# Performance work log

Measured on AMD Instinct MI355X. Metric: run time of the kernel, lower is better.

Reference implementation:

```python
import jax, jax.numpy as jnp
import numpy as np

B, T, N, D = 16, 16, 256, 384  # batch, timesteps, patches, feature dim
QDIM = 384                      # query_dim
TEMP = 1.0                      # temperature
TOPK = 16                       # topk_k
EPS = 1e-8


def setup_inputs() -> dict:
    key = jax.random.key(0)
    k1, k2, k3, k4, k5, k6 = jax.random.split(key, 6)
    queries = jax.random.normal(k1, (B, T, QDIM), dtype=jnp.float32)
    patch_features = jax.random.normal(k2, (B, T, N, D), dtype=jnp.float32)
    # encoder.query_input_proj: Linear(query_dim -> D)
    W_in = jax.random.normal(k3, (QDIM, D), dtype=jnp.float32) / np.sqrt(QDIM)
    b_in = jax.random.normal(k4, (D,), dtype=jnp.float32) * 0.01
    # encoder.query_output_proj: Linear(D -> dino_dim)
    W_out = jax.random.normal(k5, (D, QDIM), dtype=jnp.float32) / np.sqrt(D)
    b_out = jax.random.normal(k6, (QDIM,), dtype=jnp.float32) * 0.01
    return {"queries": queries, "patch_features": patch_features,
            "W_in": W_in, "b_in": b_in, "W_out": W_out, "b_out": b_out}


def reference(queries, patch_features, W_in, b_in, W_out, b_out):
    # q_proj: [B,T,D]
    q_proj = jnp.einsum('btq,qd->btd', queries, W_in) + b_in
    # scores: [B,T,N]
    scores = jnp.einsum('btd,btnd->btn', q_proj, patch_features) / TEMP
    attn = jax.nn.softmax(scores, axis=-1)
    # top-k hard mask + renormalize
    k = min(TOPK, N)
    vals, idx = jax.lax.top_k(attn, k)                     # [B,T,k]
    bi = jnp.arange(B)[:, None, None]
    ti = jnp.arange(T)[None, :, None]
    attn_hard = jnp.zeros_like(attn).at[bi, ti, idx].set(vals)
    attn = attn_hard / (attn_hard.sum(axis=-1, keepdims=True) + EPS)
    # weighted sum over patches: [B,T,D]
    out = jnp.einsum('btn,btnd->btd', attn, patch_features)
    out = jnp.einsum('btd,dq->btq', out, W_out) + b_out    # [B,T,QDIM]
    return out
```

## Files before the change

kernel.cpp:

```cpp
#include <hip/hip_runtime.h>
#include <math.h>

#define B_  16
#define T_  16
#define N_  256
#define D_  384
#define Q_  384
#define K_  16
#define BT_ (B_ * T_)

__global__ __launch_bounds__(1024, 4)
void fused_kernel(const float* __restrict__ queries,
                  const float* __restrict__ patch,
                  const float* __restrict__ W_in,
                  const float* __restrict__ b_in,
                  const float* __restrict__ W_out,
                  const float* __restrict__ b_out,
                  float* __restrict__ out)
{
    const int bt   = blockIdx.x;
    const int tid  = threadIdx.x;
    const int lane = tid & 63;
    const int wave = tid >> 6;

    __shared__ __align__(16) float s_q[Q_];
    __shared__ __align__(16) float s_qp[D_];
    __shared__ __align__(16) float s_sc[N_];
    __shared__ __align__(16) int   s_cnt4[N_][4];
    __shared__ float s_red[4];
    __shared__ float s_red2[4][2];
    __shared__ float s_w[K_];
    __shared__ int   s_ix[K_];
    __shared__ __align__(16) float s_p8[8][D_];
    __shared__ __align__(16) float s_od[D_];

    const float* __restrict__ ptile = patch + (size_t)bt * N_ * D_;
    float* s_flat = &s_p8[0][0];

    if (tid < Q_) s_q[tid] = queries[(size_t)bt * Q_ + tid];
    __syncthreads();

    const int g16 = lane >> 4;
    const int sl  = lane & 15;
    const int n0  = wave * 4 + g16;

    float4 A[6], Bu[6], C[6];

#define LOADROW(dst, it) {                                                     \
        const float* pr = ptile + (size_t)(n0 + (it) * 64) * D_;               \
        _Pragma("unroll")                                                      \
        for (int c = 0; c < 6; ++c)                                            \
            dst[c] = *reinterpret_cast<const float4*>(pr + c * 64 + 4 * sl); }

#define DOTSTORE(src, it) {                                                    \
        float p = 0.f;                                                         \
        _Pragma("unroll")                                                      \
        for (int c = 0; c < 6; ++c)                                            \
            p += src[c].x * qv[c].x + src[c].y * qv[c].y                       \
               + src[c].z * qv[c].z + src[c].w * qv[c].w;                      \
        _Pragma("unroll")                                                      \
        for (int off = 8; off; off >>= 1) p += __shfl_xor(p, off, 16);         \
        if (sl == 0) s_sc[n0 + (it) * 64] = p; }

    LOADROW(A, 0)
    LOADROW(Bu, 1)
    LOADROW(C, 2)
    __builtin_amdgcn_sched_barrier(0);

    if (tid < 768) {
        const int s = tid / 96;
        const int g = tid % 96;
        float4 acc = {0.f, 0.f, 0.f, 0.f};
        const float* wp = W_in + (size_t)(s * 48) * D_ + 4 * g;
        #pragma unroll 4
        for (int qq = 0; qq < 48; ++qq) {
            const float4 w = *reinterpret_cast<const float4*>(wp + (size_t)qq * D_);
            const float qs = s_q[s * 48 + qq];
            acc.x += qs * w.x; acc.y += qs * w.y;
            acc.z += qs * w.z; acc.w += qs * w.w;
        }
        *reinterpret_cast<float4*>(&s_p8[s][4 * g]) = acc;
    }
    __syncthreads();
    if (tid < D_) {
        float v = b_in[tid];
        #pragma unroll
        for (int s = 0; s < 8; ++s) v += s_p8[s][tid];
        s_qp[tid] = v;
    }
    __syncthreads();

    {
        const float4* s_qp4 = reinterpret_cast<const float4*>(s_qp);
        float4 qv[6];
        #pragma unroll
        for (int c = 0; c < 6; ++c) qv[c] = s_qp4[c * 16 + sl];

        DOTSTORE(A, 0)
        LOADROW(A, 3)
        DOTSTORE(Bu, 1)
        DOTSTORE(C, 2)
        DOTSTORE(A, 3)
    }
#undef LOADROW
#undef DOTSTORE
    __syncthreads();

    if (tid < N_) {
        float v = s_sc[tid];
        #pragma unroll
        for (int off = 32; off; off >>= 1) v = fmaxf(v, __shfl_xor(v, off));
        if (lane == 0) s_red[wave] = v;
    }
    {
        const int i   = tid >> 2;
        const int sub = tid & 3;
        const float si = s_sc[i];
        const float4* s_sc4 = reinterpret_cast<const float4*>(s_sc);
        int c = 0;
        #pragma unroll
        for (int jj = 0; jj < 16; ++jj) {
            const int jr = (jj + sub * 4) & 15;
            const float4 v = s_sc4[sub * 16 + jr];
            const int j0 = sub * 64 + jr * 4;
            c += (int)(v.x > si) | ((int)(v.x == si) & (int)((j0 + 0) < i));
            c += (int)(v.y > si) | ((int)(v.y == si) & (int)((j0 + 1) < i));
            c += (int)(v.z > si) | ((int)(v.z == si) & (int)((j0 + 2) < i));
            c += (int)(v.w > si) | ((int)(v.w == si) & (int)((j0 + 3) < i));
        }
        s_cnt4[i][sub] = c;
    }
    __syncthreads();

    float e = 0.f;
    int   cnt = N_;
    if (tid < N_) {
        const float mx = fmaxf(fmaxf(s_red[0], s_red[1]), fmaxf(s_red[2], s_red[3]));
        const int4 c4 = reinterpret_cast<const int4*>(s_cnt4)[tid];
        cnt = c4.x + c4.y + c4.z + c4.w;
        e = __expf(s_sc[tid] - mx);

        float z  = e;
        float sk = (cnt < K_) ? e : 0.f;
        #pragma unroll
        for (int off = 32; off; off >>= 1) {
            z  += __shfl_xor(z, off);
            sk += __shfl_xor(sk, off);
        }
        if (lane == 0) { s_red2[wave][0] = z; s_red2[wave][1] = sk; }
    }
    __syncthreads();

    {
        const float Z  = s_red2[0][0] + s_red2[1][0] + s_red2[2][0] + s_red2[3][0];
        const float SK = s_red2[0][1] + s_red2[1][1] + s_red2[2][1] + s_red2[3][1];
        const float inv = 1.f / (SK + 1e-8f * Z);
        if (tid < N_ && cnt < K_) {
            s_ix[cnt] = tid;
            s_w[cnt]  = e * inv;
        }
    }
    __syncthreads();

    if (tid < 2 * D_) {
        const int half = tid >= D_;
        const int d    = tid - half * D_;
        const int j0   = half * (K_ / 2);
        float acc = 0.f;
        #pragma unroll
        for (int j = j0; j < j0 + K_ / 2; ++j)
            acc += s_w[j] * ptile[(size_t)s_ix[j] * D_ + d];
        s_flat[tid] = acc;
    }
    __syncthreads();
    if (tid < D_) s_od[tid] = s_flat[tid] + s_flat[tid + D_];
    __syncthreads();

    if (tid < 768) {
        const int s = tid / 96;
        const int g = tid % 96;
        float4 acc = {0.f, 0.f, 0.f, 0.f};
        const float* wp = W_out + (size_t)(s * 48) * Q_ + 4 * g;
        #pragma unroll 4
        for (int dd = 0; dd < 48; ++dd) {
            const float4 w = *reinterpret_cast<const float4*>(wp + (size_t)dd * Q_);
            const float ov = s_od[s * 48 + dd];
            acc.x += ov * w.x; acc.y += ov * w.y;
            acc.z += ov * w.z; acc.w += ov * w.w;
        }
        *reinterpret_cast<float4*>(&s_p8[s][4 * g]) = acc;
    }
    __syncthreads();
    if (tid < Q_) {
        float v = b_out[tid];
        #pragma unroll
        for (int s = 0; s < 8; ++s) v += s_p8[s][tid];
        out[(size_t)bt * Q_ + tid] = v;
    }
}

extern "C" void kernel_launch(void* const* d_in, const int* in_sizes, int n_in,
                              void* d_out, int out_size, void* d_ws, size_t ws_size,
                              hipStream_t stream) {
    const float* queries = (const float*)d_in[0];
    const float* patch   = (const float*)d_in[1];
    const float* W_in    = (const float*)d_in[2];
    const float* b_in    = (const float*)d_in[3];
    const float* W_out   = (const float*)d_in[4];
    const float* b_out   = (const float*)d_in[5];
    float* out = (float*)d_out;

    fused_kernel<<<dim3(BT_), dim3(1024), 0, stream>>>(
        queries, patch, W_in, b_in, W_out, b_out, out);
}
```

Baseline: 34.46 us.

## Pack top-k rank keys, prefetch W_out during gather, single-pass weighted sum

Scores are encoded as order-preserving unsigned keys with the patch index in the low 8 bits, so the rank count uses one unsigned compare instead of a compare plus tie-break. The first eight W_out rows are prefetched into registers before the top-k gather so their latency overlaps it. The gather now runs on 384 threads with four independent accumulators, removing one shared-memory reduction and a barrier. Truncating the low 8 mantissa bits can change the selection when scores are nearly tied, and the prefetch raises register pressure.

```diff
diff --git a/kernel.cpp b/kernel.cpp
--- a/kernel.cpp
+++ b/kernel.cpp
@@ -26,6 +26,7 @@
     __shared__ __align__(16) float s_q[Q_];
     __shared__ __align__(16) float s_qp[D_];
     __shared__ __align__(16) float s_sc[N_];
+    __shared__ __align__(16) unsigned s_ku[N_];
     __shared__ __align__(16) int   s_cnt4[N_][4];
     __shared__ float s_red[4];
     __shared__ float s_red2[4][2];
@@ -35,7 +36,6 @@
     __shared__ __align__(16) float s_od[D_];
 
     const float* __restrict__ ptile = patch + (size_t)bt * N_ * D_;
-    float* s_flat = &s_p8[0][0];
 
     if (tid < Q_) s_q[tid] = queries[(size_t)bt * Q_ + tid];
     __syncthreads();
@@ -60,7 +60,13 @@
                + src[c].z * qv[c].z + src[c].w * qv[c].w;                      \
         _Pragma("unroll")                                                      \
         for (int off = 8; off; off >>= 1) p += __shfl_xor(p, off, 16);         \
-        if (sl == 0) s_sc[n0 + (it) * 64] = p; }
+        if (sl == 0) {                                                         \
+            const int nn = n0 + (it) * 64;                                     \
+            s_sc[nn] = p;                                                      \
+            const unsigned u = __float_as_uint(p);                             \
+            const unsigned ord = u ^ ((unsigned)((int)u >> 31) | 0x80000000u); \
+            s_ku[nn] = (ord & 0xFFFFFF00u) | (255u - (unsigned)nn);            \
+        } }
 
     LOADROW(A, 0)
     LOADROW(Bu, 1)
@@ -115,18 +121,15 @@
     {
         const int i   = tid >> 2;
         const int sub = tid & 3;
-        const float si = s_sc[i];
-        const float4* s_sc4 = reinterpret_cast<const float4*>(s_sc);
+        const unsigned ki = s_ku[i];
+        const uint4* k4 = reinterpret_cast<const uint4*>(s_ku);
         int c = 0;
         #pragma unroll
         for (int jj = 0; jj < 16; ++jj) {
             const int jr = (jj + sub * 4) & 15;
-            const float4 v = s_sc4[sub * 16 + jr];
-            const int j0 = sub * 64 + jr * 4;
-            c += (int)(v.x > si) | ((int)(v.x == si) & (int)((j0 + 0) < i));
-            c += (int)(v.y > si) | ((int)(v.y == si) & (int)((j0 + 1) < i));
-            c += (int)(v.z > si) | ((int)(v.z == si) & (int)((j0 + 2) < i));
-            c += (int)(v.w > si) | ((int)(v.w == si) & (int)((j0 + 3) < i));
+            const uint4 v = k4[sub * 16 + jr];
+            c += (int)(v.x > ki) + (int)(v.y > ki)
+               + (int)(v.z > ki) + (int)(v.w > ki);
         }
         s_cnt4[i][sub] = c;
     }
@@ -162,29 +165,46 @@
     }
     __syncthreads();
 
-    if (tid < 2 * D_) {
-        const int half = tid >= D_;
-        const int d    = tid - half * D_;
-        const int j0   = half * (K_ / 2);
-        float acc = 0.f;
-        #pragma unroll
-        for (int j = j0; j < j0 + K_ / 2; ++j)
-            acc += s_w[j] * ptile[(size_t)s_ix[j] * D_ + d];
-        s_flat[tid] = acc;
-    }
-    __syncthreads();
-    if (tid < D_) s_od[tid] = s_flat[tid] + s_flat[tid + D_];
-    __syncthreads();
-
+    float4 wpre[8];
+    const float* wp = W_out;
     if (tid < 768) {
         const int s = tid / 96;
         const int g = tid % 96;
+        wp = W_out + (size_t)(s * 48) * Q_ + 4 * g;
+        #pragma unroll
+        for (int p = 0; p < 8; ++p)
+            wpre[p] = *reinterpret_cast<const float4*>(wp + (size_t)p * Q_);
+    }
+    __builtin_amdgcn_sched_barrier(0);
+
+    if (tid < D_) {
+        float a0 = 0.f, a1 = 0.f, a2 = 0.f, a3 = 0.f;
+        #pragma unroll
+        for (int j = 0; j < K_; j += 4) {
+            a0 += s_w[j + 0] * ptile[(size_t)s_ix[j + 0] * D_ + tid];
+            a1 += s_w[j + 1] * ptile[(size_t)s_ix[j + 1] * D_ + tid];
+            a2 += s_w[j + 2] * ptile[(size_t)s_ix[j + 2] * D_ + tid];
+            a3 += s_w[j + 3] * ptile[(size_t)s_ix[j + 3] * D_ + tid];
+        }
+        s_od[tid] = (a0 + a1) + (a2 + a3);
+    }
+    __syncthreads();
+
+    if (tid < 768) {
+        const int s = tid / 96;
+        const int g = tid % 96;
+        const int base = s * 48;
         float4 acc = {0.f, 0.f, 0.f, 0.f};
-        const float* wp = W_out + (size_t)(s * 48) * Q_ + 4 * g;
+        #pragma unroll
+        for (int p = 0; p < 8; ++p) {
+            const float ov = s_od[base + p];
+            acc.x += ov * wpre[p].x; acc.y += ov * wpre[p].y;
+            acc.z += ov * wpre[p].z; acc.w += ov * wpre[p].w;
+        }
         #pragma unroll 4
-        for (int dd = 0; dd < 48; ++dd) {
+        for (int dd = 8; dd < 48; ++dd) {
             const float4 w = *reinterpret_cast<const float4*>(wp + (size_t)dd * Q_);
-            const float ov = s_od[s * 48 + dd];
+            const float ov = s_od[base + dd];
             acc.x += ov * w.x; acc.y += ov * w.y;
             acc.z += ov * w.z; acc.w += ov * w.w;
         }
```

Measured after the change: 32.67 us. 1.05x faster.
